# Performance work log

Measured on AMD Instinct MI355X. Metric: run time of the kernel, lower is better.

## Reference

```python
import jax, jax.numpy as jnp
import numpy as np
import math

B, N, E = 32, 512, 8192          # graphs, nodes/graph, edges/graph
IN_DIM, D, H, HD, L, C = 64, 128, 4, 32, 3, 10
HID = 2 * D                      # _FeatureMLP hidden = max(d, 2*d)


def _ln(x, g, b, eps=1e-5):
    mu = x.mean(-1, keepdims=True)
    var = ((x - mu) ** 2).mean(-1, keepdims=True)
    return (x - mu) / jnp.sqrt(var + eps) * g + b


def _gelu(x):
    return jax.nn.gelu(x, approximate=False)  # torch nn.GELU default (erf)


def setup_inputs() -> dict:
    key = jax.random.key(0)
    ks = iter(jax.random.split(key, 48))
    def w(*shape):
        return jax.random.normal(next(ks), shape, jnp.float32) * 0.02
    z = lambda *s: jnp.zeros(s, jnp.float32)
    o = lambda *s: jnp.ones(s, jnp.float32)
    return {
        'x': jax.random.normal(next(ks), (B * N, IN_DIM), jnp.float32),
        'src': jax.random.randint(next(ks), (B, E), 0, N),
        'dst': jax.random.randint(next(ks), (B, E), 0, N),
        # node encoder: Linear -> LN -> GELU -> Linear -> LN
        'enc_w1': w(IN_DIM, HID), 'enc_b1': z(HID), 'enc_g1': o(HID), 'enc_bn1': z(HID),
        'enc_w2': w(HID, D), 'enc_b2': z(D), 'enc_g2': o(D), 'enc_bn2': z(D),
        # per-layer edge-message MLP (stacked over L)
        'msg_w1': w(L, 2 * D, D), 'msg_b1': z(L, D),
        'msg_w2': w(L, D, D), 'msg_b2': z(L, D),
        'msg_g': o(L, D), 'msg_bb': z(L, D),
        # per-layer attention
        'qw': w(L, D, H * HD), 'qb': z(L, H * HD),
        'kw': w(L, D, H * HD), 'kb': z(L, H * HD),
        'vw': w(L, D, H * HD), 'vb': z(L, H * HD),
        'ow': w(L, H * HD, D), 'ob': z(L, D),
        'attn_g': o(L, D), 'attn_b': z(L, D),
        # graph head: Linear(4d,2d) -> GELU -> LN -> Linear(2d,C)
        'gh_w1': w(4 * D, 2 * D), 'gh_b1': z(2 * D),
        'gh_g': o(2 * D), 'gh_bn': z(2 * D),
        'gh_w2': w(2 * D, C), 'gh_b2': z(C),
    }


def reference(x, src, dst, enc_w1, enc_b1, enc_g1, enc_bn1, enc_w2, enc_b2, enc_g2, enc_bn2,
              msg_w1, msg_b1, msg_w2, msg_b2, msg_g, msg_bb,
              qw, qb, kw, kb, vw, vb, ow, ob, attn_g, attn_b,
              gh_w1, gh_b1, gh_g, gh_bn, gh_w2, gh_b2):
    # node encoder
    t = _ln(x @ enc_w1 + enc_b1, enc_g1, enc_bn1)
    h = _ln(_gelu(t) @ enc_w2 + enc_b2, enc_g2, enc_bn2)
    h = h.reshape(B, N, D)
    seg = jax.vmap(lambda m, d: jax.ops.segment_sum(m, d, num_segments=N))
    for l in range(L):
        # edge message block: gather src/dst, MLP, scatter-add to dst
        hs = jnp.take_along_axis(h, src[..., None], axis=1)   # [B,E,D]
        hd = jnp.take_along_axis(h, dst[..., None], axis=1)   # [B,E,D]
        m = _gelu(jnp.concatenate([hs, hd], -1) @ msg_w1[l] + msg_b1[l]) @ msg_w2[l] + msg_b2[l]
        h = _ln(h + seg(m, dst), msg_g[l], msg_bb[l])
        # masked attention block (dense per-graph attention)
        q = (h @ qw[l] + qb[l]).reshape(B, N, H, HD)
        k = (h @ kw[l] + kb[l]).reshape(B, N, H, HD)
        v = (h @ vw[l] + vb[l]).reshape(B, N, H, HD)
        scores = jnp.einsum('bnhd,bmhd->bhnm', q, k) / math.sqrt(HD)
        attn = jax.nn.softmax(scores, axis=-1)
        o = jnp.einsum('bhnm,bmhd->bnhd', attn, v).reshape(B, N, H * HD)
        h = _ln(h + o @ ow[l] + ob[l], attn_g[l], attn_b[l])
    # graph pooling: mean | sum | max | std
    mean = h.mean(1)
    summ = h.sum(1)
    mx = h.max(1)
    std = jnp.sqrt(jax.nn.relu((h ** 2).mean(1) - mean ** 2) + 1e-6)
    pool = jnp.concatenate([mean, summ, mx, std], -1)         # [B,4D]
    g = _ln(_gelu(pool @ gh_w1 + gh_b1), gh_g, gh_bn)
    return g @ gh_w2 + gh_b2                                   # [B,C]
```

## Files before the change

kernel.cpp:

```cpp
#include <hip/hip_runtime.h>
#include <cmath>

#define B_   32
#define N_   512
#define E_   8192
#define BN_  16384
#define D_   128

typedef short bf16x8 __attribute__((ext_vector_type(8)));
typedef float f32x4  __attribute__((ext_vector_type(4)));

static __device__ __forceinline__ float bf2f(unsigned short u){
  union{unsigned int i; float f;} v; v.i = ((unsigned int)u)<<16; return v.f;
}
static __device__ __forceinline__ unsigned short f2bf(float f){
  union{unsigned int i; float f;} v; v.f=f;
  unsigned int x=v.i;
  return (unsigned short)((x + 0x7fffu + ((x>>16)&1u))>>16);
}
static __device__ __forceinline__ unsigned int pack2(float a, float b){
  return (unsigned int)f2bf(a) | ((unsigned int)f2bf(b)<<16);
}
static __device__ __forceinline__ float gelu_f(float x){
  float xs=x*0.70710678118654752f;
  float ax=fabsf(xs);
  float t=__builtin_amdgcn_rcpf(1.0f+0.3275911f*ax);
  float p=t*(0.254829592f+t*(-0.284496736f+t*(1.421413741f+t*(-1.453152027f+t*1.061405429f))));
  float er=1.0f - p*__expf(-ax*ax);
  er = (xs<0.f)? -er : er;
  return 0.5f*x*(1.0f+er);
}
static __device__ __forceinline__ float gelu_t(float x){
  float x2=x*x;
  float y=x*(-1.5957691216f + x2*(-0.0713548162f));
  float e=__expf(y);
  return x*__builtin_amdgcn_rcpf(1.0f+e);
}
static __device__ __forceinline__ float ldin(const void* p, size_t i, int isbf){
  return isbf ? bf2f(((const unsigned short*)p)[i]) : ((const float*)p)[i];
}

static __device__ __forceinline__ void block_sum2(float a, float b, float&A, float&Bv, float* red, int nw){
  int lane=threadIdx.x&63, w=threadIdx.x>>6;
  #pragma unroll
  for(int o=32;o>0;o>>=1){ a+=__shfl_down(a,o); b+=__shfl_down(b,o); }
  if(lane==0){ red[w]=a; red[8+w]=b; }
  __syncthreads();
  float sa=0.f, sb=0.f;
  for(int i=0;i<nw;i++){ sa+=red[i]; sb+=red[8+i]; }
  __syncthreads();
  A=sa; Bv=sb;
}

__global__ void sniff_kernel(const unsigned int* __restrict__ xw, int* __restrict__ flag){
  int t=threadIdx.x;
  int cnt=0;
  for(int i=0;i<32;i++){
    unsigned int w=xw[t+64*i];
    float v=bf2f((unsigned short)(w&0xffffu));
    float av=fabsf(v);
    if(v==0.0f || (av>=6e-5f && av<=8.0f)) cnt++;
  }
  #pragma unroll
  for(int o=32;o>0;o>>=1) cnt+=__shfl_down(cnt,o);
  if(t==0) *flag=(cnt>=1024)?1:0;
}

__global__ __launch_bounds__(256) void count_kernel(
  const int* __restrict__ dst, int* __restrict__ cnt)
{
  __shared__ int lc[512];
  int g=blockIdx.x, c=blockIdx.y, t=threadIdx.x;
  for(int i=t;i<512;i+=256) lc[i]=0;
  __syncthreads();
  for(int e=t;e<1024;e+=256) atomicAdd(&lc[dst[(size_t)g*E_+c*1024+e]],1);
  __syncthreads();
  for(int i=t;i<512;i+=256){ int v=lc[i]; if(v) atomicAdd(&cnt[g*512+i],v); }
}

__global__ __launch_bounds__(256) void scan_kernel(
  int* __restrict__ cnt, int* __restrict__ rowptr)
{
  __shared__ int sc[512];
  int g=blockIdx.x, t=threadIdx.x;
  for(int i=t;i<512;i+=256) sc[i]=cnt[g*512+i];
  __syncthreads();
  if(t==0){
    int acc=0;
    for(int i=0;i<512;i++){ int c=sc[i]; rowptr[g*513+i]=acc; cnt[g*512+i]=acc; acc+=c; }
    rowptr[g*513+512]=acc;
  }
}

__global__ __launch_bounds__(256) void scatter_kernel(
  const int* __restrict__ src, const int* __restrict__ dst,
  int* __restrict__ off, unsigned short* __restrict__ ss)
{
  int g=blockIdx.x, c=blockIdx.y, t=threadIdx.x;
  for(int e=t;e<1024;e+=256){
    size_t idx=(size_t)g*E_+c*1024+e;
    int d=dst[idx];
    int pos=atomicAdd(&off[g*512+d],1);
    ss[(size_t)g*E_+pos]=(unsigned short)src[idx];
  }
}

__global__ __launch_bounds__(256) void prep_kernel(
  const void* __restrict__ msg_w1, const void* __restrict__ msg_w2,
  const void* __restrict__ qw, const void* __restrict__ kw,
  const void* __restrict__ vw, const void* __restrict__ ow,
  const void* __restrict__ qb, const void* __restrict__ kb, const void* __restrict__ vb,
  const void* __restrict__ ob, const void* __restrict__ msg_b1, const void* __restrict__ msg_b2,
  const void* __restrict__ msg_g, const void* __restrict__ msg_bb,
  const void* __restrict__ attn_g, const void* __restrict__ attn_b,
  const void* __restrict__ enc_w1, const void* __restrict__ enc_w2,
  const void* __restrict__ enc_b1, const void* __restrict__ enc_g1, const void* __restrict__ enc_bn1,
  const void* __restrict__ enc_b2, const void* __restrict__ enc_g2, const void* __restrict__ enc_bn2,
  const void* __restrict__ gh_w1, const void* __restrict__ gh_w2,
  const void* __restrict__ gh_b1, const void* __restrict__ gh_g,
  const void* __restrict__ gh_bn, const void* __restrict__ gh_b2,
  unsigned short* __restrict__ w1t, unsigned short* __restrict__ w2k,
  unsigned short* __restrict__ qkvt, unsigned short* __restrict__ owt,
  unsigned short* __restrict__ w1te, unsigned short* __restrict__ w2te,
  unsigned short* __restrict__ ghw1t, unsigned short* __restrict__ ghw2t,
  unsigned short* __restrict__ cb, const int* __restrict__ flag)
{
  int isbf=*flag;
  int job=blockIdx.y;
  int i=blockIdx.x*256+threadIdx.x;
  if(job<3){
    if(i<32768){ int l=job; int k=i>>7, n=i&127; w1t[l*32768 + n*256 + k]=f2bf(ldin(msg_w1,(size_t)l*32768+i,isbf)); }
  } else if(job<6){
    int l=job-3; if(i<16384){ w2k[l*16384 + i]=f2bf(ldin(msg_w2,(size_t)l*16384+i,isbf)); }
  } else if(job<15){
    int r=job-6, l=r/3, which=r%3;
    if(i<16384){ int k=i>>7, n=i&127;
      const void* w=(which==0)?qw:((which==1)?kw:vw);
      qkvt[l*49152 + (which*128+n)*128 + k]=f2bf(ldin(w,(size_t)l*16384+i,isbf)); }
  } else if(job<18){
    int l=job-15; if(i<16384){ int k=i>>7, n=i&127; owt[l*16384 + n*128 + k]=f2bf(ldin(ow,(size_t)l*16384+i,isbf)); }
  } else if(job==18){
    if(i<3840){
      float v;
      if(i<1152){ int l=i/384, j=i%384, which=j>>7, jj=j&127;
        const void* bb=(which==0)?qb:((which==1)?kb:vb);
        v=ldin(bb,(size_t)l*128+jj,isbf);
      } else {
        int i2=i-1152; int r=i2/384; int rem=i2%384;
        const void* s = (r==0)?ob:((r==1)?msg_b1:((r==2)?msg_b2:((r==3)?msg_g:((r==4)?msg_bb:((r==5)?attn_g:attn_b)))));
        v=ldin(s,(size_t)rem,isbf);
      }
      cb[i]=f2bf(v);
    }
  } else if(job==19){
    if(i<1152){
      float v;
      if(i<256)       v=ldin(enc_b1,i,isbf);
      else if(i<512)  v=ldin(enc_g1,i-256,isbf);
      else if(i<768)  v=ldin(enc_bn1,i-512,isbf);
      else if(i<896)  v=ldin(enc_b2,i-768,isbf);
      else if(i<1024) v=ldin(enc_g2,i-896,isbf);
      else            v=ldin(enc_bn2,i-1024,isbf);
      cb[3840+i]=f2bf(v);
    }
  } else if(job==20){
    if(i<16384){ int k=i>>8, n=i&255; w1te[n*64+k]=f2bf(ldin(enc_w1,(size_t)i,isbf)); }
  } else if(job==21){
    if(i<32768){ int k=i>>7, n=i&127; w2te[n*256+k]=f2bf(ldin(enc_w2,(size_t)i,isbf)); }
  } else if(job<26){
    int p=job-22; int j=p*32768+i;
    if(i<32768){ int k=j>>8, n=j&255; ghw1t[n*512+k]=f2bf(ldin(gh_w1,(size_t)j,isbf)); }
  } else {
    if(i<2560){ int k=i/10, n=i%10; ghw2t[n*256+k]=f2bf(ldin(gh_w2,(size_t)i,isbf)); }
    else if(i<2560+778){
      int j=i-2560; float v;
      if(j<256)      v=ldin(gh_b1,j,isbf);
      else if(j<512) v=ldin(gh_g,j-256,isbf);
      else if(j<768) v=ldin(gh_bn,j-512,isbf);
      else           v=ldin(gh_b2,j-768,isbf);
      cb[4992+j]=f2bf(v);
    }
  }
}

__global__ __launch_bounds__(256) void enc_kernel(
  const void* __restrict__ x, const unsigned short* __restrict__ w1te,
  const unsigned short* __restrict__ w2te, const unsigned short* __restrict__ cb,
  unsigned short* __restrict__ h, const int* __restrict__ flag)
{
  __shared__ __align__(16) unsigned short xs[64][72];
  __shared__ __align__(16) unsigned short t1[64][264];
  int isbf=*flag;
  int m0=blockIdx.x*64;
  int t=threadIdx.x, lane=t&63, w=t>>6, quad=lane>>4, ln=lane&15;
  for(int c2=t;c2<1024;c2+=256){
    int i=c2*4, row=i>>6, col=i&63;
    float v0,v1,v2,v3;
    if(isbf){
      const unsigned short* p=(const unsigned short*)x+(size_t)m0*64+i;
      v0=bf2f(p[0]); v1=bf2f(p[1]); v2=bf2f(p[2]); v3=bf2f(p[3]);
    } else {
      float4 f=*(const float4*)((const float*)x+(size_t)m0*64+i);
      v0=f.x; v1=f.y; v2=f.z; v3=f.w;
    }
    ushort4 o; o.x=f2bf(v0); o.y=f2bf(v1); o.z=f2bf(v2); o.w=f2bf(v3);
    *(ushort4*)&xs[row][col]=o;
  }
  __syncthreads();
  f32x4 a[4][4];
  #pragma unroll
  for(int nt=0;nt<4;nt++){ a[nt][0]={0,0,0,0}; a[nt][1]={0,0,0,0}; a[nt][2]={0,0,0,0}; a[nt][3]={0,0,0,0}; }
  #pragma unroll
  for(int k0i=0;k0i<2;k0i++){
    bf16x8 af[4];
    #pragma unroll
    for(int f=0;f<4;f++) af[f]=*(const bf16x8*)(&xs[f*16+ln][k0i*32+quad*8]);
    #pragma unroll
    for(int nt=0;nt<4;nt++){
      int n=w*64+nt*16+ln;
      bf16x8 bfr=*(const bf16x8*)(w1te+(size_t)n*64+k0i*32+quad*8);
      #pragma unroll
      for(int f=0;f<4;f++) a[nt][f]=__builtin_amdgcn_mfma_f32_16x16x32_bf16(af[f],bfr,a[nt][f],0,0,0);
    }
  }
  #pragma unroll
  for(int nt=0;nt<4;nt++){
    int n=w*64+nt*16+ln;
    float bv=bf2f(cb[3840+n]);
    #pragma unroll
    for(int f=0;f<4;f++)
      #pragma unroll
      for(int r=0;r<4;r++) t1[f*16+quad*4+r][n]=f2bf(a[nt][f][r]+bv);
  }
  __syncthreads();
  {
    int row=t>>2, qq=t&3;
    float s=0.f,s2=0.f;
    for(int c=qq*64;c<qq*64+64;c++){ float v=bf2f(t1[row][c]); s+=v; s2+=v*v; }
    s+=__shfl_xor(s,1); s+=__shfl_xor(s,2);
    s2+=__shfl_xor(s2,1); s2+=__shfl_xor(s2,2);
    float mu=s*(1.f/256.f), var=fmaxf(s2*(1.f/256.f)-mu*mu,0.f);
    float rr=rsqrtf(var+1e-5f);
    for(int c=qq*64;c<qq*64+64;c++){
      float v=bf2f(t1[row][c]);
      t1[row][c]=f2bf(gelu_f((v-mu)*rr*bf2f(cb[4096+c])+bf2f(cb[4352+c])));
    }
  }
  __syncthreads();
  f32x4 b2a[2][4];
  #pragma unroll
  for(int nt=0;nt<2;nt++){ b2a[nt][0]={0,0,0,0}; b2a[nt][1]={0,0,0,0}; b2a[nt][2]={0,0,0,0}; b2a[nt][3]={0,0,0,0}; }
  #pragma unroll
  for(int k0i=0;k0i<8;k0i++){
    bf16x8 af[4];
    #pragma unroll
    for(int f=0;f<4;f++) af[f]=*(const bf16x8*)(&t1[f*16+ln][k0i*32+quad*8]);
    #pragma unroll
    for(int nt=0;nt<2;nt++){
      int n=w*32+nt*16+ln;
      bf16x8 bfr=*(const bf16x8*)(w2te+(size_t)n*256+k0i*32+quad*8);
      #pragma unroll
      for(int f=0;f<4;f++) b2a[nt][f]=__builtin_amdgcn_mfma_f32_16x16x32_bf16(af[f],bfr,b2a[nt][f],0,0,0);
    }
  }
  __syncthreads();
  float* mf=(float*)&t1[0][0];
  #pragma unroll
  for(int nt=0;nt<2;nt++){
    int n=w*32+nt*16+ln;
    float bv=bf2f(cb[4608+n]);
    #pragma unroll
    for(int f=0;f<4;f++)
      #pragma unroll
      for(int r=0;r<4;r++) mf[(f*16+quad*4+r)*132+n]=b2a[nt][f][r]+bv;
  }
  __syncthreads();
  {
    int row=t>>2, qq=t&3;
    float s=0.f,s2=0.f;
    for(int c=qq*32;c<qq*32+32;c++){ float v=mf[row*132+c]; s+=v; s2+=v*v; }
    s+=__shfl_xor(s,1); s+=__shfl_xor(s,2);
    s2+=__shfl_xor(s2,1); s2+=__shfl_xor(s2,2);
    float mu=s*(1.f/128.f), var=fmaxf(s2*(1.f/128.f)-mu*mu,0.f);
    float rr=rsqrtf(var+1e-5f);
    for(int c=qq*32;c<qq*32+32;c+=2){
      float v0=(mf[row*132+c  ]-mu)*rr*bf2f(cb[4736+c  ])+bf2f(cb[4864+c  ]);
      float v1=(mf[row*132+c+1]-mu)*rr*bf2f(cb[4736+c+1])+bf2f(cb[4864+c+1]);
      *(unsigned int*)(h+(size_t)(m0+row)*128+c)=pack2(v0,v1);
    }
  }
}

__global__ __launch_bounds__(256) void uvgen_kernel(
  const unsigned short* __restrict__ hrows, const unsigned short* __restrict__ w1t,
  const unsigned short* __restrict__ b1, unsigned short* __restrict__ UV)
{
  __shared__ __align__(16) unsigned short a_t[64][136];
  int t=threadIdx.x;
  int m0=blockIdx.x*64;
  int y=blockIdx.y;
  for(int c=t;c<1024;c+=256){
    int m=c>>4, pp=c&15;
    *(uint4*)&a_t[m][pp*8]=*((const uint4*)(hrows+(size_t)(m0+m)*128)+pp);
  }
  __syncthreads();
  int lane=t&63, w=t>>6, quad=lane>>4, ln=lane&15;
  #pragma unroll
  for(int nt=0;nt<2;nt++){
    int n=w*32+nt*16+ln;
    f32x4 a0={0,0,0,0},a1={0,0,0,0},a2={0,0,0,0},a3={0,0,0,0};
    const unsigned short* wp=w1t+(size_t)n*256+y*128+quad*8;
    #pragma unroll
    for(int k0=0;k0<128;k0+=32){
      bf16x8 bfr=*(const bf16x8*)(wp+k0);
      bf16x8 f0=*(const bf16x8*)(&a_t[ln   ][k0+quad*8]);
      bf16x8 f1=*(const bf16x8*)(&a_t[16+ln][k0+quad*8]);
      bf16x8 f2=*(const bf16x8*)(&a_t[32+ln][k0+quad*8]);
      bf16x8 f3=*(const bf16x8*)(&a_t[48+ln][k0+quad*8]);
      a0=__builtin_amdgcn_mfma_f32_16x16x32_bf16(f0,bfr,a0,0,0,0);
      a1=__builtin_amdgcn_mfma_f32_16x16x32_bf16(f1,bfr,a1,0,0,0);
      a2=__builtin_amdgcn_mfma_f32_16x16x32_bf16(f2,bfr,a2,0,0,0);
      a3=__builtin_amdgcn_mfma_f32_16x16x32_bf16(f3,bfr,a3,0,0,0);
    }
    float bv=y?0.f:bf2f(b1[n]);
    #pragma unroll
    for(int r2=0;r2<4;r2++){
      UV[(size_t)(m0+quad*4+r2   )*256+y*128+n]=f2bf(a0[r2]+bv);
      UV[(size_t)(m0+16+quad*4+r2)*256+y*128+n]=f2bf(a1[r2]+bv);
      UV[(size_t)(m0+32+quad*4+r2)*256+y*128+n]=f2bf(a2[r2]+bv);
      UV[(size_t)(m0+48+quad*4+r2)*256+y*128+n]=f2bf(a3[r2]+bv);
    }
  }
}

__global__ __launch_bounds__(128) void edgef_kernel(
  unsigned short* __restrict__ h,
  const unsigned short* __restrict__ UV,
  const unsigned short* __restrict__ ss,
  const int* __restrict__ rowptr,
  const unsigned short* __restrict__ w2k,
  const unsigned short* __restrict__ b2,
  const unsigned short* __restrict__ gg, const unsigned short* __restrict__ bbp,
  int b0, int gEp)
{
  __shared__ __align__(16) float aggL[2][4][128];
  __shared__ __align__(16) float po[2][4][128];
  int t=threadIdx.x, lane=t&63, w=t>>6;
  int bid=blockIdx.x;
  int lg=bid%gEp, ch=bid/gEp;
  int g=b0+lg;
  const unsigned short* UVg = UV + (size_t)lg*512*256;
  const unsigned short* ssg = ss + (size_t)g*E_;
  int dbase = ch*4;
  int bnd[5];
  #pragma unroll
  for(int i=0;i<5;i++) bnd[i]=rowptr[g*513+dbase+i];
  #pragma unroll 1
  for(int dd=0;dd<4;dd++){
    int e_lo=bnd[dd], e_hi0=bnd[dd+1];
    int half=(e_hi0-e_lo+1)>>1;
    int es = w ? (e_lo+half) : e_lo;
    int ee = w ? e_hi0       : (e_lo+half);
    unsigned int vdw=*(const unsigned int*)(UVg + (size_t)(dbase+dd)*256 + 128 + lane*2);
    float v0=bf2f((unsigned short)(vdw&0xffffu)), v1=bf2f((unsigned short)(vdw>>16));
    float a0=0.f, a1=0.f;
    int si3,si4,si5;
    unsigned int u0,u1,u2;
    {
      int s0=__builtin_amdgcn_readfirstlane((int)ssg[es  ])&511;
      int s1=__builtin_amdgcn_readfirstlane((int)ssg[es+1])&511;
      int s2=__builtin_amdgcn_readfirstlane((int)ssg[es+2])&511;
      si3=(int)ssg[es+3]; si4=(int)ssg[es+4]; si5=(int)ssg[es+5];
      u0=*(const unsigned int*)(UVg + (size_t)s0*256 + lane*2);
      u1=*(const unsigned int*)(UVg + (size_t)s1*256 + lane*2);
      u2=*(const unsigned int*)(UVg + (size_t)s2*256 + lane*2);
    }
    #pragma unroll 2
    for(int e=es;e<ee;e++){
      float z0=bf2f((unsigned short)(u0&0xffffu))+v0;
      float z1=bf2f((unsigned short)(u0>>16))+v1;
      u0=u1; u1=u2;
      int s3=__builtin_amdgcn_readfirstlane(si3)&511;
      u2=*(const unsigned int*)(UVg + (size_t)s3*256 + lane*2);
      si3=si4; si4=si5;
      si5=(int)ssg[e+6];
      a0+=gelu_t(z0); a1+=gelu_t(z1);
    }
    aggL[w][dd][lane*2  ]=a0;
    aggL[w][dd][lane*2+1]=a1;
  }
  __syncthreads();
  float o[4][2];
  #pragma unroll
  for(int dd=0;dd<4;dd++){ o[dd][0]=0.f; o[dd][1]=0.f; }
  #pragma unroll 4
  for(int kk=0;kk<64;kk++){
    int k=w*64+kk;
    unsigned int wdw=*(const unsigned int*)(w2k+(size_t)k*128+lane*2);
    float w0=bf2f((unsigned short)(wdw&0xffffu));
    float w1=bf2f((unsigned short)(wdw>>16));
    #pragma unroll
    for(int dd=0;dd<4;dd++){
      float av=aggL[0][dd][k]+aggL[1][dd][k];
      o[dd][0]+=av*w0; o[dd][1]+=av*w1;
    }
  }
  #pragma unroll
  for(int dd=0;dd<4;dd++){
    po[w][dd][lane*2  ]=o[dd][0];
    po[w][dd][lane*2+1]=o[dd][1];
  }
  __syncthreads();
  #pragma unroll 1
  for(int p=0;p<2;p++){
    int di=w*2+p;
    int d = dbase + di;
    float deg=(float)(bnd[di+1]-bnd[di]);
    float o0=bf2f(b2[lane*2  ])*deg + po[0][di][lane*2  ] + po[1][di][lane*2  ];
    float o1=bf2f(b2[lane*2+1])*deg + po[0][di][lane*2+1] + po[1][di][lane*2+1];
    size_t base=(size_t)(g*512+d)*128;
    unsigned int hdw=*(const unsigned int*)(h+base+lane*2);
    float x0=bf2f((unsigned short)(hdw&0xffffu))+o0;
    float x1=bf2f((unsigned short)(hdw>>16))+o1;
    float s1=x0+x1, s2=x0*x0+x1*x1;
    #pragma unroll
    for(int off=32;off>0;off>>=1){ s1+=__shfl_xor(s1,off); s2+=__shfl_xor(s2,off); }
    float mu=s1*(1.f/128.f), var=fmaxf(s2*(1.f/128.f)-mu*mu,0.f);
    float rr=rsqrtf(var+1e-5f);
    float y0=(x0-mu)*rr*bf2f(gg[lane*2  ])+bf2f(bbp[lane*2  ]);
    float y1=(x1-mu)*rr*bf2f(gg[lane*2+1])+bf2f(bbp[lane*2+1]);
    *(unsigned int*)(h+base+lane*2)=pack2(y0,y1);
  }
}

__global__ __launch_bounds__(256) void attnf_kernel(
  const unsigned short* __restrict__ h, const unsigned short* __restrict__ wqkv,
  const unsigned short* __restrict__ bq, unsigned short* __restrict__ obuf, int b0, int gA)
{
  __shared__ __align__(16) unsigned short Qs[128][40];
  __shared__ __align__(16) unsigned short Ks[64][72];
  __shared__ __align__(16) unsigned short Vts[32][72];
  __shared__ __align__(16) unsigned short Ps[64][72];
  int bx=blockIdx.x;
  int lg=bx%gA; int rr2=bx/gA; int hh=rr2&3, qq4=rr2>>2;
  int g=b0+lg;
  int t=threadIdx.x, lane=t&63, w=t>>6, quad=lane>>4, ln=lane&15;
  const unsigned short* hg=h+(size_t)g*512*128;
  const float sc=0.17677669529663689f;
  bf16x8 wk[2][4], wv[2][4];
  #pragma unroll
  for(int nt=0;nt<2;nt++)
    #pragma unroll
    for(int k0i=0;k0i<4;k0i++){
      int n=hh*32+nt*16+ln;
      wk[nt][k0i]=*(const bf16x8*)(wqkv+(size_t)(128+n)*128+k0i*32+quad*8);
      wv[nt][k0i]=*(const bf16x8*)(wqkv+(size_t)(256+n)*128+k0i*32+quad*8);
    }
  #pragma unroll
  for(int qt=0;qt<2;qt++){
    int r0=qq4*128+qt*64+w*16;
    bf16x8 af[4];
    #pragma unroll
    for(int k0i=0;k0i<4;k0i++) af[k0i]=*(const bf16x8*)(hg+(size_t)(r0+ln)*128+k0i*32+quad*8);
    #pragma unroll
    for(int nt=0;nt<2;nt++){
      int dim=nt*16+ln;
      f32x4 c={0,0,0,0};
      #pragma unroll
      for(int k0i=0;k0i<4;k0i++){
        bf16x8 bfr=*(const bf16x8*)(wqkv+(size_t)(hh*32+dim)*128+k0i*32+quad*8);
        c=__builtin_amdgcn_mfma_f32_16x16x32_bf16(af[k0i],bfr,c,0,0,0);
      }
      float bv=bf2f(bq[hh*32+dim]);
      #pragma unroll
      for(int r=0;r<4;r++) Qs[qt*64+w*16+quad*4+r][dim]=f2bf((c[r]+bv)*sc);
    }
  }
  f32x4 O[2][2]; float Lp[2][4];
  #pragma unroll
  for(int qt=0;qt<2;qt++){ O[qt][0]={0,0,0,0}; O[qt][1]={0,0,0,0};
    #pragma unroll
    for(int r=0;r<4;r++) Lp[qt][r]=0.f; }
  for(int kc=0;kc<8;kc++){
    __syncthreads();
    {
      int r0=kc*64+w*16;
      bf16x8 af[4];
      #pragma unroll
      for(int k0i=0;k0i<4;k0i++) af[k0i]=*(const bf16x8*)(hg+(size_t)(r0+ln)*128+k0i*32+quad*8);
      #pragma unroll
      for(int nt=0;nt<2;nt++){
        int dim=nt*16+ln;
        f32x4 ck={0,0,0,0}, cv={0,0,0,0};
        #pragma unroll
        for(int k0i=0;k0i<4;k0i++){
          ck=__builtin_amdgcn_mfma_f32_16x16x32_bf16(af[k0i],wk[nt][k0i],ck,0,0,0);
          cv=__builtin_amdgcn_mfma_f32_16x16x32_bf16(af[k0i],wv[nt][k0i],cv,0,0,0);
        }
        float bk=bf2f(bq[128+hh*32+dim]), bv2=bf2f(bq[256+hh*32+dim]);
        #pragma unroll
        for(int r=0;r<4;r++){
          int key=w*16+quad*4+r;
          Ks[key][dim]=f2bf(ck[r]+bk);
          Vts[dim][key]=f2bf(cv[r]+bv2);
        }
      }
    }
    __syncthreads();
    #pragma unroll
    for(int qt=0;qt<2;qt++){
      bf16x8 qf=*(const bf16x8*)(&Qs[qt*64+w*16+ln][quad*8]);
      f32x4 s[4];
      #pragma unroll
      for(int f=0;f<4;f++){
        bf16x8 kf=*(const bf16x8*)(&Ks[f*16+ln][quad*8]);
        f32x4 z={0,0,0,0};
        s[f]=__builtin_amdgcn_mfma_f32_16x16x32_bf16(qf,kf,z,0,0,0);
      }
      #pragma unroll
      for(int f=0;f<4;f++)
        #pragma unroll
        for(int r=0;r<4;r++){
          float pe=__expf(fminf(s[f][r],30.0f));
          Ps[w*16+quad*4+r][f*16+ln]=f2bf(pe);
          Lp[qt][r]+=pe;
        }
      #pragma unroll
      for(int s2=0;s2<2;s2++){
        bf16x8 pf=*(const bf16x8*)(&Ps[w*16+ln][s2*32+quad*8]);
        bf16x8 v0=*(const bf16x8*)(&Vts[ln   ][s2*32+quad*8]);
        bf16x8 v1=*(const bf16x8*)(&Vts[16+ln][s2*32+quad*8]);
        O[qt][0]=__builtin_amdgcn_mfma_f32_16x16x32_bf16(pf,v0,O[qt][0],0,0,0);
        O[qt][1]=__builtin_amdgcn_mfma_f32_16x16x32_bf16(pf,v1,O[qt][1],0,0,0);
      }
    }
  }
  #pragma unroll
  for(int qt=0;qt<2;qt++){
    #pragma unroll
    for(int o=1;o<16;o<<=1)
      #pragma unroll
      for(int r=0;r<4;r++) Lp[qt][r]+=__shfl_xor(Lp[qt][r],o);
    #pragma unroll
    for(int r=0;r<4;r++){
      float inv=1.0f/Lp[qt][r];
      size_t row=(size_t)lg*512+qq4*128+qt*64+w*16+quad*4+r;
      obuf[row*128+hh*32+ln   ]=f2bf(O[qt][0][r]*inv);
      obuf[row*128+hh*32+16+ln]=f2bf(O[qt][1][r]*inv);
    }
  }
}

__global__ __launch_bounds__(256) void oproj_kernel(
  const unsigned short* __restrict__ obuf, const unsigned short* __restrict__ wo,
  const unsigned short* __restrict__ bo, unsigned short* __restrict__ h,
  const unsigned short* __restrict__ gg, const unsigned short* __restrict__ bbp, int b0)
{
  __shared__ __align__(16) unsigned short a_t[64][136];
  __shared__ float mf[64][132];
  int t=threadIdx.x, lane=t&63, w=t>>6, quad=lane>>4, ln=lane&15;
  int m0=blockIdx.x*64;
  for(int c=t;c<64*16;c+=256){
    int m=c>>4, pp=c&15;
    *(uint4*)&a_t[m][pp*8]=*((const uint4*)(obuf+(size_t)(m0+m)*128)+pp);
  }
  __syncthreads();
  #pragma unroll
  for(int nt=0;nt<2;nt++){
    int n=w*32+nt*16+ln;
    f32x4 a0={0,0,0,0},a1={0,0,0,0},a2={0,0,0,0},a3={0,0,0,0};
    const unsigned short* wp=wo+(size_t)n*128+quad*8;
    #pragma unroll
    for(int k0=0;k0<128;k0+=32){
      bf16x8 bfr=*(const bf16x8*)(wp+k0);
      bf16x8 f0=*(const bf16x8*)(&a_t[ln   ][k0+quad*8]);
      bf16x8 f1=*(const bf16x8*)(&a_t[16+ln][k0+quad*8]);
      bf16x8 f2=*(const bf16x8*)(&a_t[32+ln][k0+quad*8]);
      bf16x8 f3=*(const bf16x8*)(&a_t[48+ln][k0+quad*8]);
      a0=__builtin_amdgcn_mfma_f32_16x16x32_bf16(f0,bfr,a0,0,0,0);
      a1=__builtin_amdgcn_mfma_f32_16x16x32_bf16(f1,bfr,a1,0,0,0);
      a2=__builtin_amdgcn_mfma_f32_16x16x32_bf16(f2,bfr,a2,0,0,0);
      a3=__builtin_amdgcn_mfma_f32_16x16x32_bf16(f3,bfr,a3,0,0,0);
    }
    float bv=bf2f(bo[n]);
    #pragma unroll
    for(int r=0;r<4;r++){
      mf[quad*4+r   ][n]=a0[r]+bv;
      mf[16+quad*4+r][n]=a1[r]+bv;
      mf[32+quad*4+r][n]=a2[r]+bv;
      mf[48+quad*4+r][n]=a3[r]+bv;
    }
  }
  __syncthreads();
  {
    int row=t>>2, qq=t&3;
    size_t base=(size_t)(b0*512+m0+row)*128;
    float s=0.f,s2=0.f;
    float vals[32];
    for(int j=0;j<32;j++){
      int c=qq*32+j;
      float v=bf2f(h[base+c])+mf[row][c];
      vals[j]=v; s+=v; s2+=v*v;
    }
    s+=__shfl_xor(s,1); s+=__shfl_xor(s,2);
    s2+=__shfl_xor(s2,1); s2+=__shfl_xor(s2,2);
    float mu=s*(1.f/128.f), var=fmaxf(s2*(1.f/128.f)-mu*mu,0.f);
    float rr=rsqrtf(var+1e-5f);
    for(int j=0;j<32;j+=2){
      int c=qq*32+j;
      float v0=(vals[j]  -mu)*rr*bf2f(gg[c  ])+bf2f(bbp[c  ]);
      float v1=(vals[j+1]-mu)*rr*bf2f(gg[c+1])+bf2f(bbp[c+1]);
      *(unsigned int*)(h+base+c)=pack2(v0,v1);
    }
  }
}

__global__ __launch_bounds__(256) void poolp_kernel(
  const unsigned short* __restrict__ h, float* __restrict__ part)
{
  __shared__ float ps[256], ps2[256], pm[256];
  int b=blockIdx.x, c=blockIdx.y;
  int t=threadIdx.x, d=t&127, hf=t>>7;
  float s=0.f,s2=0.f,mx=-1e30f;
  for(int r=hf*32;r<hf*32+32;r++){
    float v=bf2f(h[((size_t)(b*512+c*64+r))*128+d]);
    s+=v; s2+=v*v; mx=fmaxf(mx,v);
  }
  ps[t]=s; ps2[t]=s2; pm[t]=mx;
  __syncthreads();
  if(t<128){
    s=ps[t]+ps[128+t]; s2=ps2[t]+ps2[128+t]; mx=fmaxf(pm[t],pm[128+t]);
    size_t base=((size_t)(b*8+c))*384;
    part[base+t]=s; part[base+128+t]=s2; part[base+256+t]=mx;
  }
}

__global__ __launch_bounds__(256) void head_kernel(
  const float* __restrict__ part, const unsigned short* __restrict__ ghw1t,
  const unsigned short* __restrict__ ghw2t, const unsigned short* __restrict__ cb,
  void* __restrict__ out, const int* __restrict__ flag)
{
  int isbf=*flag;
  int b=blockIdx.x, t=threadIdx.x;
  __shared__ float pl[512];
  __shared__ float gl[256];
  __shared__ float red[16];
  if(t<128){
    float s=0.f,s2=0.f,mx=-1e30f;
    for(int c=0;c<8;c++){
      size_t base=((size_t)(b*8+c))*384;
      s += part[base+t];
      s2+= part[base+128+t];
      mx = fmaxf(mx, part[base+256+t]);
    }
    float mean=s*(1.f/512.f);
    float var=fmaxf(s2*(1.f/512.f)-mean*mean,0.f);
    float sd=sqrtf(var+1e-6f);
    pl[t]=mean; pl[128+t]=s; pl[256+t]=mx; pl[384+t]=sd;
  }
  __syncthreads();
  float a=bf2f(cb[4992+t]);
  const unsigned short* wr=ghw1t+(size_t)t*512;
  for(int k0=0;k0<512;k0+=8){
    bf16x8 wv=*(const bf16x8*)(wr+k0);
    const unsigned short* wp=(const unsigned short*)&wv;
    #pragma unroll
    for(int j=0;j<8;j++) a+=pl[k0+j]*bf2f(wp[j]);
  }
  float u=gelu_f(a);
  float S,S2; block_sum2(u,u*u,S,S2,red,4);
  float mu=S*(1.f/256.f), var=fmaxf(S2*(1.f/256.f)-mu*mu,0.f);
  float r=rsqrtf(var+1e-5f);
  gl[t]=(u-mu)*r*bf2f(cb[5248+t])+bf2f(cb[5504+t]);
  __syncthreads();
  if(t<10){
    float o=bf2f(cb[5760+t]);
    const unsigned short* wr2=ghw2t+(size_t)t*256;
    for(int k0=0;k0<256;k0+=8){
      bf16x8 wv=*(const bf16x8*)(wr2+k0);
      const unsigned short* wp=(const unsigned short*)&wv;
      #pragma unroll
      for(int j=0;j<8;j++) o+=gl[k0+j]*bf2f(wp[j]);
    }
    if(isbf) ((unsigned short*)out)[b*10+t]=f2bf(o);
    else     ((float*)out)[b*10+t]=o;
  }
}

extern "C" void kernel_launch(void* const* d_in, const int* in_sizes, int n_in,
                              void* d_out, int out_size, void* d_ws, size_t ws_size,
                              hipStream_t stream)
{
  const void* x      =d_in[0];
  const int*  src    =(const int*)d_in[1];
  const int*  dstp   =(const int*)d_in[2];
  const void* enc_w1 =d_in[3];  const void* enc_b1 =d_in[4];
  const void* enc_g1 =d_in[5];  const void* enc_bn1=d_in[6];
  const void* enc_w2 =d_in[7];  const void* enc_b2 =d_in[8];
  const void* enc_g2 =d_in[9];  const void* enc_bn2=d_in[10];
  const void* msg_w1 =d_in[11]; const void* msg_b1 =d_in[12];
  const void* msg_w2 =d_in[13]; const void* msg_b2 =d_in[14];
  const void* msg_g  =d_in[15]; const void* msg_bb =d_in[16];
  const void* qw     =d_in[17]; const void* qb     =d_in[18];
  const void* kw     =d_in[19]; const void* kb     =d_in[20];
  const void* vw     =d_in[21]; const void* vb     =d_in[22];
  const void* ow     =d_in[23]; const void* ob     =d_in[24];
  const void* attn_g =d_in[25]; const void* attn_b =d_in[26];
  const void* gh_w1  =d_in[27]; const void* gh_b1  =d_in[28];
  const void* gh_g   =d_in[29]; const void* gh_bn  =d_in[30];
  const void* gh_w2  =d_in[31]; const void* gh_b2  =d_in[32];
  (void)in_sizes; (void)n_in; (void)out_size;

  const size_t MB=1024*1024;
  char* base=(char*)d_ws;
  unsigned short* h    =(unsigned short*)(base);
  unsigned short* w1t  =(unsigned short*)(base + 4194304);
  unsigned short* w2k  =(unsigned short*)(base + 4390912);
  unsigned short* qkvt =(unsigned short*)(base + 4489216);
  unsigned short* owt  =(unsigned short*)(base + 4784128);
  unsigned short* w1te =(unsigned short*)(base + 4882432);
  unsigned short* w2te =(unsigned short*)(base + 4915200);
  unsigned short* ghw1t=(unsigned short*)(base + 4980736);
  unsigned short* ghw2t=(unsigned short*)(base + 5242880);
  unsigned short* cb   =(unsigned short*)(base + 5248000);
  int*   rowptr        =(int*)(base + 5325312);
  int*   flag          =(int*)(base + 5390976);
  int*   cnt           =(int*)(base + 5391360);
  unsigned short* ssrt =(unsigned short*)(base + 5505024);
  char* R              = base + 6029312;

  int epass, apass;
  if(ws_size >= (size_t)(14.5*MB)){ epass=1; apass=1; }
  else if(ws_size >= 10*MB){ epass=2; apass=1; }
  else { epass=4; apass=2; }
  int gEp=B_/epass, gA=B_/apass;
  int rowsA=gA*512;
  float* part=(float*)R;

  sniff_kernel<<<1,64,0,stream>>>((const unsigned int*)x, flag);
  hipMemsetAsync(cnt,0,65536,stream);
  count_kernel<<<dim3(B_,8),256,0,stream>>>(dstp,cnt);
  scan_kernel<<<B_,256,0,stream>>>(cnt,rowptr);
  scatter_kernel<<<dim3(B_,8),256,0,stream>>>(src,dstp,cnt,ssrt);
  prep_kernel<<<dim3(128,27),256,0,stream>>>(msg_w1,msg_w2,qw,kw,vw,ow,qb,kb,vb,
      ob,msg_b1,msg_b2,msg_g,msg_bb,attn_g,attn_b,
      enc_w1,enc_w2,enc_b1,enc_g1,enc_bn1,enc_b2,enc_g2,enc_bn2,
      gh_w1,gh_w2,gh_b1,gh_g,gh_bn,gh_b2,
      w1t,w2k,qkvt,owt,w1te,w2te,ghw1t,ghw2t,cb,flag);

  enc_kernel<<<BN_/64,256,0,stream>>>(x,w1te,w2te,cb,h,flag);

  for(int l=0;l<3;l++){
    for(int ep=0;ep<epass;ep++){
      int b0=ep*gEp;
      unsigned short* UV=(unsigned short*)R;
      uvgen_kernel<<<dim3(gEp*8,2),256,0,stream>>>(h+(size_t)b0*512*128,
          w1t+(size_t)l*32768, cb+1536+l*128, UV);
      edgef_kernel<<<gEp*128,128,0,stream>>>(h,UV,ssrt,rowptr,
          w2k+(size_t)l*16384, cb+1920+l*128, cb+2304+l*128, cb+2688+l*128, b0, gEp);
    }
    for(int ap=0;ap<apass;ap++){
      int b0=ap*gA;
      unsigned short* obuf=(unsigned short*)R;
      attnf_kernel<<<gA*16,256,0,stream>>>(h, qkvt+(size_t)l*49152, cb+l*384, obuf, b0, gA);
      oproj_kernel<<<rowsA/64,256,0,stream>>>(obuf, owt+(size_t)l*16384,
          cb+1152+l*128, h, cb+3072+l*128, cb+3456+l*128, b0);
    }
  }
  poolp_kernel<<<dim3(B_,8),256,0,stream>>>(h,part);
  head_kernel<<<B_,256,0,stream>>>(part,ghw1t,ghw2t,cb,d_out,flag);
}
```

Before: 435.4 us.

## Use atomic work queue in edge kernel and merge uvgen column halves

The edge aggregation kernel now launches half as many blocks. Each block repeatedly takes a 4-node chunk of its graph from a per-graph atomic counter, so blocks that drew low-degree nodes pick up more work and skew in degrees evens out. The uvgen kernel computes both the U and V halves (256 output columns) in one block instead of two grid.y slices, so each block stages the A tile in LDS once instead of twice. The trade-offs are more accumulators per thread, extra atomics and barriers per chunk, and a larger memset to zero the queue counters.

Measured after the change: 518.3 us. 19.0% more time.

```diff
diff --git a/kernel.cpp b/kernel.cpp
--- a/kernel.cpp
+++ b/kernel.cpp
@@ -298,38 +298,40 @@
   __shared__ __align__(16) unsigned short a_t[64][136];
   int t=threadIdx.x;
   int m0=blockIdx.x*64;
-  int y=blockIdx.y;
   for(int c=t;c<1024;c+=256){
     int m=c>>4, pp=c&15;
     *(uint4*)&a_t[m][pp*8]=*((const uint4*)(hrows+(size_t)(m0+m)*128)+pp);
   }
   __syncthreads();
   int lane=t&63, w=t>>6, quad=lane>>4, ln=lane&15;
-  #pragma unroll
-  for(int nt=0;nt<2;nt++){
-    int n=w*32+nt*16+ln;
-    f32x4 a0={0,0,0,0},a1={0,0,0,0},a2={0,0,0,0},a3={0,0,0,0};
-    const unsigned short* wp=w1t+(size_t)n*256+y*128+quad*8;
-    #pragma unroll
-    for(int k0=0;k0<128;k0+=32){
-      bf16x8 bfr=*(const bf16x8*)(wp+k0);
-      bf16x8 f0=*(const bf16x8*)(&a_t[ln   ][k0+quad*8]);
-      bf16x8 f1=*(const bf16x8*)(&a_t[16+ln][k0+quad*8]);
-      bf16x8 f2=*(const bf16x8*)(&a_t[32+ln][k0+quad*8]);
-      bf16x8 f3=*(const bf16x8*)(&a_t[48+ln][k0+quad*8]);
-      a0=__builtin_amdgcn_mfma_f32_16x16x32_bf16(f0,bfr,a0,0,0,0);
-      a1=__builtin_amdgcn_mfma_f32_16x16x32_bf16(f1,bfr,a1,0,0,0);
-      a2=__builtin_amdgcn_mfma_f32_16x16x32_bf16(f2,bfr,a2,0,0,0);
-      a3=__builtin_amdgcn_mfma_f32_16x16x32_bf16(f3,bfr,a3,0,0,0);
-    }
-    float bv=y?0.f:bf2f(b1[n]);
-    #pragma unroll
-    for(int r2=0;r2<4;r2++){
-      UV[(size_t)(m0+quad*4+r2   )*256+y*128+n]=f2bf(a0[r2]+bv);
-      UV[(size_t)(m0+16+quad*4+r2)*256+y*128+n]=f2bf(a1[r2]+bv);
-      UV[(size_t)(m0+32+quad*4+r2)*256+y*128+n]=f2bf(a2[r2]+bv);
-      UV[(size_t)(m0+48+quad*4+r2)*256+y*128+n]=f2bf(a3[r2]+bv);
-    }
+  f32x4 a[4][4];
+  #pragma unroll
+  for(int nt=0;nt<4;nt++){ a[nt][0]={0,0,0,0}; a[nt][1]={0,0,0,0}; a[nt][2]={0,0,0,0}; a[nt][3]={0,0,0,0}; }
+  #pragma unroll
+  for(int k0i=0;k0i<4;k0i++){
+    bf16x8 af[4];
+    #pragma unroll
+    for(int f=0;f<4;f++) af[f]=*(const bf16x8*)(&a_t[f*16+ln][k0i*32+quad*8]);
+    #pragma unroll
+    for(int nt=0;nt<4;nt++){
+      int c=w*64+nt*16+ln;
+      const unsigned short* wp = (c<128)
+        ? (w1t+(size_t)c*256       + k0i*32+quad*8)
+        : (w1t+(size_t)(c-128)*256 + 128 + k0i*32+quad*8);
+      bf16x8 bfr=*(const bf16x8*)wp;
+      #pragma unroll
+      for(int f=0;f<4;f++) a[nt][f]=__builtin_amdgcn_mfma_f32_16x16x32_bf16(af[f],bfr,a[nt][f],0,0,0);
+    }
+  }
+  #pragma unroll
+  for(int nt=0;nt<4;nt++){
+    int c=w*64+nt*16+ln;
+    float bv=(c<128)?bf2f(b1[c]):0.f;
+    #pragma unroll
+    for(int f=0;f<4;f++)
+      #pragma unroll
+      for(int r=0;r<4;r++)
+        UV[(size_t)(m0+f*16+quad*4+r)*256 + c]=f2bf(a[nt][f][r]+bv);
   }
 }
 
@@ -341,95 +343,101 @@
   const unsigned short* __restrict__ w2k,
   const unsigned short* __restrict__ b2,
   const unsigned short* __restrict__ gg, const unsigned short* __restrict__ bbp,
-  int b0, int gEp)
+  int* __restrict__ qc, int b0, int gEp)
 {
   __shared__ __align__(16) float aggL[2][4][128];
   __shared__ __align__(16) float po[2][4][128];
+  __shared__ int chs;
   int t=threadIdx.x, lane=t&63, w=t>>6;
-  int bid=blockIdx.x;
-  int lg=bid%gEp, ch=bid/gEp;
+  int lg=blockIdx.x%gEp;
   int g=b0+lg;
   const unsigned short* UVg = UV + (size_t)lg*512*256;
   const unsigned short* ssg = ss + (size_t)g*E_;
-  int dbase = ch*4;
-  int bnd[5];
-  #pragma unroll
-  for(int i=0;i<5;i++) bnd[i]=rowptr[g*513+dbase+i];
-  #pragma unroll 1
-  for(int dd=0;dd<4;dd++){
-    int e_lo=bnd[dd], e_hi0=bnd[dd+1];
-    int half=(e_hi0-e_lo+1)>>1;
-    int es = w ? (e_lo+half) : e_lo;
-    int ee = w ? e_hi0       : (e_lo+half);
-    unsigned int vdw=*(const unsigned int*)(UVg + (size_t)(dbase+dd)*256 + 128 + lane*2);
-    float v0=bf2f((unsigned short)(vdw&0xffffu)), v1=bf2f((unsigned short)(vdw>>16));
-    float a0=0.f, a1=0.f;
-    int si3,si4,si5;
-    unsigned int u0,u1,u2;
-    {
-      int s0=__builtin_amdgcn_readfirstlane((int)ssg[es  ])&511;
-      int s1=__builtin_amdgcn_readfirstlane((int)ssg[es+1])&511;
-      int s2=__builtin_amdgcn_readfirstlane((int)ssg[es+2])&511;
-      si3=(int)ssg[es+3]; si4=(int)ssg[es+4]; si5=(int)ssg[es+5];
-      u0=*(const unsigned int*)(UVg + (size_t)s0*256 + lane*2);
-      u1=*(const unsigned int*)(UVg + (size_t)s1*256 + lane*2);
-      u2=*(const unsigned int*)(UVg + (size_t)s2*256 + lane*2);
-    }
-    #pragma unroll 2
-    for(int e=es;e<ee;e++){
-      float z0=bf2f((unsigned short)(u0&0xffffu))+v0;
-      float z1=bf2f((unsigned short)(u0>>16))+v1;
-      u0=u1; u1=u2;
-      int s3=__builtin_amdgcn_readfirstlane(si3)&511;
-      u2=*(const unsigned int*)(UVg + (size_t)s3*256 + lane*2);
-      si3=si4; si4=si5;
-      si5=(int)ssg[e+6];
-      a0+=gelu_t(z0); a1+=gelu_t(z1);
-    }
-    aggL[w][dd][lane*2  ]=a0;
-    aggL[w][dd][lane*2+1]=a1;
-  }
-  __syncthreads();
-  float o[4][2];
-  #pragma unroll
-  for(int dd=0;dd<4;dd++){ o[dd][0]=0.f; o[dd][1]=0.f; }
-  #pragma unroll 4
-  for(int kk=0;kk<64;kk++){
-    int k=w*64+kk;
-    unsigned int wdw=*(const unsigned int*)(w2k+(size_t)k*128+lane*2);
-    float w0=bf2f((unsigned short)(wdw&0xffffu));
-    float w1=bf2f((unsigned short)(wdw>>16));
-    #pragma unroll
+  for(;;){
+    if(t==0) chs=atomicAdd(&qc[lg],1);
+    __syncthreads();
+    int ch=chs;
+    if(ch>=128) break;
+    int dbase = ch*4;
+    int bnd[5];
+    #pragma unroll
+    for(int i=0;i<5;i++) bnd[i]=rowptr[g*513+dbase+i];
+    #pragma unroll 1
     for(int dd=0;dd<4;dd++){
-      float av=aggL[0][dd][k]+aggL[1][dd][k];
-      o[dd][0]+=av*w0; o[dd][1]+=av*w1;
-    }
-  }
-  #pragma unroll
-  for(int dd=0;dd<4;dd++){
-    po[w][dd][lane*2  ]=o[dd][0];
-    po[w][dd][lane*2+1]=o[dd][1];
-  }
-  __syncthreads();
-  #pragma unroll 1
-  for(int p=0;p<2;p++){
-    int di=w*2+p;
-    int d = dbase + di;
-    float deg=(float)(bnd[di+1]-bnd[di]);
-    float o0=bf2f(b2[lane*2  ])*deg + po[0][di][lane*2  ] + po[1][di][lane*2  ];
-    float o1=bf2f(b2[lane*2+1])*deg + po[0][di][lane*2+1] + po[1][di][lane*2+1];
-    size_t base=(size_t)(g*512+d)*128;
-    unsigned int hdw=*(const unsigned int*)(h+base+lane*2);
-    float x0=bf2f((unsigned short)(hdw&0xffffu))+o0;
-    float x1=bf2f((unsigned short)(hdw>>16))+o1;
-    float s1=x0+x1, s2=x0*x0+x1*x1;
-    #pragma unroll
-    for(int off=32;off>0;off>>=1){ s1+=__shfl_xor(s1,off); s2+=__shfl_xor(s2,off); }
-    float mu=s1*(1.f/128.f), var=fmaxf(s2*(1.f/128.f)-mu*mu,0.f);
-    float rr=rsqrtf(var+1e-5f);
-    float y0=(x0-mu)*rr*bf2f(gg[lane*2  ])+bf2f(bbp[lane*2  ]);
-    float y1=(x1-mu)*rr*bf2f(gg[lane*2+1])+bf2f(bbp[lane*2+1]);
-    *(unsigned int*)(h+base+lane*2)=pack2(y0,y1);
+      int e_lo=bnd[dd], e_hi0=bnd[dd+1];
+      int half=(e_hi0-e_lo+1)>>1;
+      int es = w ? (e_lo+half) : e_lo;
+      int ee = w ? e_hi0       : (e_lo+half);
+      unsigned int vdw=*(const unsigned int*)(UVg + (size_t)(dbase+dd)*256 + 128 + lane*2);
+      float v0=bf2f((unsigned short)(vdw&0xffffu)), v1=bf2f((unsigned short)(vdw>>16));
+      float a0=0.f, a1=0.f;
+      int si3,si4,si5;
+      unsigned int u0,u1,u2;
+      {
+        int s0=__builtin_amdgcn_readfirstlane((int)ssg[es  ])&511;
+        int s1=__builtin_amdgcn_readfirstlane((int)ssg[es+1])&511;
+        int s2=__builtin_amdgcn_readfirstlane((int)ssg[es+2])&511;
+        si3=(int)ssg[es+3]; si4=(int)ssg[es+4]; si5=(int)ssg[es+5];
+        u0=*(const unsigned int*)(UVg + (size_t)s0*256 + lane*2);
+        u1=*(const unsigned int*)(UVg + (size_t)s1*256 + lane*2);
+        u2=*(const unsigned int*)(UVg + (size_t)s2*256 + lane*2);
+      }
+      #pragma unroll 2
+      for(int e=es;e<ee;e++){
+        float z0=bf2f((unsigned short)(u0&0xffffu))+v0;
+        float z1=bf2f((unsigned short)(u0>>16))+v1;
+        u0=u1; u1=u2;
+        int s3=__builtin_amdgcn_readfirstlane(si3)&511;
+        u2=*(const unsigned int*)(UVg + (size_t)s3*256 + lane*2);
+        si3=si4; si4=si5;
+        si5=(int)ssg[e+6];
+        a0+=gelu_t(z0); a1+=gelu_t(z1);
+      }
+      aggL[w][dd][lane*2  ]=a0;
+      aggL[w][dd][lane*2+1]=a1;
+    }
+    __syncthreads();
+    float o[4][2];
+    #pragma unroll
+    for(int dd=0;dd<4;dd++){ o[dd][0]=0.f; o[dd][1]=0.f; }
+    #pragma unroll 4
+    for(int kk=0;kk<64;kk++){
+      int k=w*64+kk;
+      unsigned int wdw=*(const unsigned int*)(w2k+(size_t)k*128+lane*2);
+      float w0=bf2f((unsigned short)(wdw&0xffffu));
+      float w1=bf2f((unsigned short)(wdw>>16));
+      #pragma unroll
+      for(int dd=0;dd<4;dd++){
+        float av=aggL[0][dd][k]+aggL[1][dd][k];
+        o[dd][0]+=av*w0; o[dd][1]+=av*w1;
+      }
+    }
+    #pragma unroll
+    for(int dd=0;dd<4;dd++){
+      po[w][dd][lane*2  ]=o[dd][0];
+      po[w][dd][lane*2+1]=o[dd][1];
+    }
+    __syncthreads();
+    #pragma unroll 1
+    for(int p=0;p<2;p++){
+      int di=w*2+p;
+      int d = dbase + di;
+      float deg=(float)(bnd[di+1]-bnd[di]);
+      float o0=bf2f(b2[lane*2  ])*deg + po[0][di][lane*2  ] + po[1][di][lane*2  ];
+      float o1=bf2f(b2[lane*2+1])*deg + po[0][di][lane*2+1] + po[1][di][lane*2+1];
+      size_t base=(size_t)(g*512+d)*128;
+      unsigned int hdw=*(const unsigned int*)(h+base+lane*2);
+      float x0=bf2f((unsigned short)(hdw&0xffffu))+o0;
+      float x1=bf2f((unsigned short)(hdw>>16))+o1;
+      float s1=x0+x1, s2=x0*x0+x1*x1;
+      #pragma unroll
+      for(int off=32;off>0;off>>=1){ s1+=__shfl_xor(s1,off); s2+=__shfl_xor(s2,off); }
+      float mu=s1*(1.f/128.f), var=fmaxf(s2*(1.f/128.f)-mu*mu,0.f);
+      float rr=rsqrtf(var+1e-5f);
+      float y0=(x0-mu)*rr*bf2f(gg[lane*2  ])+bf2f(bbp[lane*2  ]);
+      float y1=(x1-mu)*rr*bf2f(gg[lane*2+1])+bf2f(bbp[lane*2+1]);
+      *(unsigned int*)(h+base+lane*2)=pack2(y0,y1);
+    }
   }
 }
 
@@ -726,6 +734,7 @@
   int*   rowptr        =(int*)(base + 5325312);
   int*   flag          =(int*)(base + 5390976);
   int*   cnt           =(int*)(base + 5391360);
+  int*   qctr          =(int*)(base + 5456896);
   unsigned short* ssrt =(unsigned short*)(base + 5505024);
   char* R              = base + 6029312;
 
@@ -738,7 +747,7 @@
   float* part=(float*)R;
 
   sniff_kernel<<<1,64,0,stream>>>((const unsigned int*)x, flag);
-  hipMemsetAsync(cnt,0,65536,stream);
+  hipMemsetAsync(cnt,0,65536+1536,stream);
   count_kernel<<<dim3(B_,8),256,0,stream>>>(dstp,cnt);
   scan_kernel<<<B_,256,0,stream>>>(cnt,rowptr);
   scatter_kernel<<<dim3(B_,8),256,0,stream>>>(src,dstp,cnt,ssrt);
@@ -753,11 +762,13 @@
   for(int l=0;l<3;l++){
     for(int ep=0;ep<epass;ep++){
       int b0=ep*gEp;
+      int slot=l*epass+ep;
       unsigned short* UV=(unsigned short*)R;
-      uvgen_kernel<<<dim3(gEp*8,2),256,0,stream>>>(h+(size_t)b0*512*128,
+      uvgen_kernel<<<gEp*8,256,0,stream>>>(h+(size_t)b0*512*128,
           w1t+(size_t)l*32768, cb+1536+l*128, UV);
-      edgef_kernel<<<gEp*128,128,0,stream>>>(h,UV,ssrt,rowptr,
-          w2k+(size_t)l*16384, cb+1920+l*128, cb+2304+l*128, cb+2688+l*128, b0, gEp);
+      edgef_kernel<<<gEp*64,128,0,stream>>>(h,UV,ssrt,rowptr,
+          w2k+(size_t)l*16384, cb+1920+l*128, cb+2304+l*128, cb+2688+l*128,
+          qctr+slot*32, b0, gEp);
     }
     for(int ap=0;ap<apass;ap++){
       int b0=ap*gA;
```
